# Kernel tuning notes

Hardware: AMD Instinct MI355X
Metric: run time of the kernel (lower is better)

The kernel has to match this reference:

```python
import jax, jax.numpy as jnp
import numpy as np

B, N, IN_DIM, SLOT_DIM, NUM_SLOTS, NUM_ITERS = 64, 4096, 256, 256, 8, 3
LN_EPS = 1e-5


def _ln(x, g, b):
    m = jnp.mean(x, axis=-1, keepdims=True)
    v = jnp.mean(jnp.square(x - m), axis=-1, keepdims=True)
    return (x - m) * jax.lax.rsqrt(v + LN_EPS) * g + b


def setup_inputs() -> dict:
    key = jax.random.key(0)
    ks = jax.random.split(key, 16)
    D, I = SLOT_DIM, IN_DIM
    s = 0.02
    return {
        "inputs": jax.random.normal(ks[0], (B, N, I), jnp.float32),
        "slots_noise": jax.random.normal(ks[1], (B, NUM_SLOTS, D), jnp.float32),
        "slots_mu": jax.random.normal(ks[2], (1, 1, D), jnp.float32),
        "slots_log_sigma": jnp.zeros((1, 1, D), jnp.float32),
        "ln_in_g": jnp.ones((I,), jnp.float32), "ln_in_b": jnp.zeros((I,), jnp.float32),
        "ln_s_g": jnp.ones((D,), jnp.float32), "ln_s_b": jnp.zeros((D,), jnp.float32),
        "ln_m_g": jnp.ones((D,), jnp.float32), "ln_m_b": jnp.zeros((D,), jnp.float32),
        "Wq": jax.random.normal(ks[3], (D, D), jnp.float32) * s,
        "Wk": jax.random.normal(ks[4], (I, D), jnp.float32) * s,
        "Wv": jax.random.normal(ks[5], (I, D), jnp.float32) * s,
        "gru_w_ih": jax.random.normal(ks[6], (3 * D, D), jnp.float32) * s,
        "gru_w_hh": jax.random.normal(ks[7], (3 * D, D), jnp.float32) * s,
        "gru_b_ih": jnp.zeros((3 * D,), jnp.float32),
        "gru_b_hh": jnp.zeros((3 * D,), jnp.float32),
        "mlp_w1": jax.random.normal(ks[8], (D, 4 * D), jnp.float32) * s,
        "mlp_b1": jnp.zeros((4 * D,), jnp.float32),
        "mlp_w2": jax.random.normal(ks[9], (4 * D, D), jnp.float32) * s,
        "mlp_b2": jnp.zeros((D,), jnp.float32),
    }


def reference(inputs, slots_noise, slots_mu, slots_log_sigma, ln_in_g, ln_in_b,
              ln_s_g, ln_s_b, ln_m_g, ln_m_b, Wq, Wk, Wv,
              gru_w_ih, gru_w_hh, gru_b_ih, gru_b_hh,
              mlp_w1, mlp_b1, mlp_w2, mlp_b2):
    D = SLOT_DIM
    # slot init: mu + sigma * noise
    slots = slots_mu + jnp.exp(slots_log_sigma) * slots_noise  # [B, S, D]
    x = _ln(inputs, ln_in_g, ln_in_b)                          # [B, N, I]
    k = x @ Wk                                                 # [B, N, D]
    v = x @ Wv                                                 # [B, N, D]
    scale = 1.0 / jnp.sqrt(jnp.float32(D))
    attn = None
    for _ in range(NUM_ITERS):
        slots_prev = slots
        s_n = _ln(slots, ln_s_g, ln_s_b)
        q = s_n @ Wq                                           # [B, S, D]
        logits = jnp.einsum('bnd,bmd->bnm', k, q) * scale      # [B, N, S]
        attn = jax.nn.softmax(logits, axis=-1)                 # softmax over slots
        attn_nrm = attn / (jnp.sum(attn, axis=1, keepdims=True) + 1e-8)
        updates = jnp.einsum('bnm,bnd->bmd', attn_nrm, v)      # [B, S, D]
        # GRUCell (PyTorch semantics)
        gi = updates @ gru_w_ih.T + gru_b_ih                   # [B, S, 3D]
        gh = slots_prev @ gru_w_hh.T + gru_b_hh
        gi_r, gi_z, gi_n = jnp.split(gi, 3, axis=-1)
        gh_r, gh_z, gh_n = jnp.split(gh, 3, axis=-1)
        r = jax.nn.sigmoid(gi_r + gh_r)
        z = jax.nn.sigmoid(gi_z + gh_z)
        n = jnp.tanh(gi_n + r * gh_n)
        slots = (1.0 - z) * n + z * slots_prev
        # residual MLP
        h = jax.nn.relu(_ln(slots, ln_m_g, ln_m_b) @ mlp_w1 + mlp_b1)
        slots = slots + h @ mlp_w2 + mlp_b2
    return slots, jnp.transpose(attn, (0, 2, 1))
```

## Files before the change

### kernel.cpp

```cpp
#include <hip/hip_runtime.h>


typedef unsigned short u16;
typedef __attribute__((ext_vector_type(8))) short bf16x8;
typedef __attribute__((ext_vector_type(4))) float f32x4;

#define MFMA16(a, b, c) __builtin_amdgcn_mfma_f32_16x16x32_bf16((a), (b), (c), 0, 0, 0)

__device__ __forceinline__ u16 f2bf(float f) {
  union { float f; unsigned u; } v; v.f = f;
  unsigned r = (v.u + 0x7fffu + ((v.u >> 16) & 1u)) >> 16;
  return (u16)r;
}
__device__ __forceinline__ float sigm(float x) { return 1.f / (1.f + __expf(-x)); }
__device__ __forceinline__ float tanh_f(float x) { return 1.f - 2.f / (1.f + __expf(2.f * x)); }

__global__ __launch_bounds__(256) void prep_kernel(
    const float* __restrict__ Wq, const float* __restrict__ Wk, const float* __restrict__ Wv,
    const float* __restrict__ wih, const float* __restrict__ whh,
    const float* __restrict__ w1, const float* __restrict__ w2,
    u16* __restrict__ wkB, u16* __restrict__ wqT, u16* __restrict__ wvT,
    u16* __restrict__ wihB, u16* __restrict__ whhB, u16* __restrict__ w1T, u16* __restrict__ w2T) {
  const int bid = blockIdx.x;
  const int tid = threadIdx.x;
  if (bid < 160) {
    __shared__ float tile[64][65];
    const float* src; u16* dst; int R, C, t;
    if (bid < 16)      { src = Wq; dst = wqT; R = 256;  C = 256;  t = bid; }
    else if (bid < 32) { src = Wv; dst = wvT; R = 256;  C = 256;  t = bid - 16; }
    else if (bid < 96) { src = w1; dst = w1T; R = 1024; C = 256;  t = bid - 32; }
    else               { src = w2; dst = w2T; R = 256;  C = 1024; t = bid - 96; }
    const int tilesJ = C >> 6;
    const int i0 = (t / tilesJ) * 64, j0 = (t % tilesJ) * 64;
    const int c = tid & 63, r0 = tid >> 6;
#pragma unroll
    for (int rr = 0; rr < 16; rr++) {
      int row = rr * 4 + r0;
      tile[row][c] = src[(size_t)(j0 + row) * R + i0 + c];
    }
    __syncthreads();
#pragma unroll
    for (int rr = 0; rr < 16; rr++) {
      int row = rr * 4 + r0;
      dst[(size_t)(i0 + row) * C + j0 + c] = f2bf(tile[c][row]);
    }
  } else {
    int gid = (bid - 160) * 256 + tid;
    for (int i4 = gid; i4 < 114688; i4 += 64 * 256) {
      int i = i4 * 4;
      const float* s; u16* d; int off;
      if (i < 65536) { s = Wk; d = wkB; off = i; }
      else if (i < 262144) { s = wih; d = wihB; off = i - 65536; }
      else { s = whh; d = whhB; off = i - 262144; }
      float4 v = *reinterpret_cast<const float4*>(s + off);
      unsigned lo = (unsigned)f2bf(v.x) | ((unsigned)f2bf(v.y) << 16);
      unsigned hi = (unsigned)f2bf(v.z) | ((unsigned)f2bf(v.w) << 16);
      *reinterpret_cast<uint2*>(d + off) = make_uint2(lo, hi);
    }
  }
}

__device__ __forceinline__ void ln_row16(const float (*src)[264], u16 (*dst)[264],
                                         const float* __restrict__ g, const float* __restrict__ bb,
                                         int wave, int lane) {
  int row = wave;
  if (row < 8) {
    float4 v = *reinterpret_cast<const float4*>(&src[row][lane * 4]);
    float s = v.x + v.y + v.z + v.w;
    float sq = v.x * v.x + v.y * v.y + v.z * v.z + v.w * v.w;
#pragma unroll
    for (int m = 1; m < 64; m <<= 1) { s += __shfl_xor(s, m); sq += __shfl_xor(sq, m); }
    float mu = s * (1.f / 256.f);
    float var = sq * (1.f / 256.f) - mu * mu;
    float rstd = rsqrtf(fmaxf(var, 0.f) + 1e-5f);
    float4 gg = *reinterpret_cast<const float4*>(&g[lane * 4]);
    float4 bv = *reinterpret_cast<const float4*>(&bb[lane * 4]);
    unsigned lo = (unsigned)f2bf((v.x - mu) * rstd * gg.x + bv.x) |
                  ((unsigned)f2bf((v.y - mu) * rstd * gg.y + bv.y) << 16);
    unsigned hi = (unsigned)f2bf((v.z - mu) * rstd * gg.z + bv.z) |
                  ((unsigned)f2bf((v.w - mu) * rstd * gg.w + bv.w) << 16);
    *reinterpret_cast<uint2*>(&dst[row][lane * 4]) = make_uint2(lo, hi);
  } else if (row < 16) {
    *reinterpret_cast<uint2*>(&dst[row][lane * 4]) = make_uint2(0, 0);
  }
}

__global__ __launch_bounds__(1024, 4) void slot_kernel(
    float* __restrict__ slots, u16* __restrict__ qg, float* __restrict__ cd,
    const float* __restrict__ wsY, const float* __restrict__ wsS,
    const u16* __restrict__ wvT, const u16* __restrict__ wihB, const u16* __restrict__ whhB,
    const u16* __restrict__ w1T, const u16* __restrict__ w2T, const u16* __restrict__ wqT,
    const u16* __restrict__ wkB,
    const float* __restrict__ bih, const float* __restrict__ bhh,
    const float* __restrict__ b1v, const float* __restrict__ b2v,
    const float* __restrict__ g_in, const float* __restrict__ b_in,
    const float* __restrict__ g_s, const float* __restrict__ b_s,
    const float* __restrict__ g_m, const float* __restrict__ b_m,
    const float* __restrict__ s_mu, const float* __restrict__ s_ls,
    const float* __restrict__ noise,
    float* __restrict__ d_out, int do_update) {
  __shared__ alignas(16) char pool[58368];
  u16 (*h_lds)[1032] = reinterpret_cast<u16(*)[1032]>(pool);
  u16 (*u_lds)[264] = reinterpret_cast<u16(*)[264]>(pool);
  u16 (*uv_lds)[264] = reinterpret_cast<u16(*)[264]>(pool + 8448);
  u16 (*sb_lds)[264] = reinterpret_cast<u16(*)[264]>(pool + 16896);
  u16 (*m_lds)[264] = reinterpret_cast<u16(*)[264]>(pool + 33024);
  float (*ns_lds)[264] = reinterpret_cast<float(*)[264]>(pool + 41472);
  u16 (*q_lds)[264] = reinterpret_cast<u16(*)[264]>(pool + 41472);
  __shared__ float sS0[16], sS1[16], sInv[16];
  __shared__ float redq[16][4][4][2];

  const int b = blockIdx.x;
  const int tid = threadIdx.x;
  const int lane = tid & 63, wave = tid >> 6;
  const int quad = lane >> 4, col = lane & 15;
  const int i256 = tid & 255, s4 = tid >> 8;
  const f32x4 vzero = {0.f, 0.f, 0.f, 0.f};

  if (do_update) {
    if (tid < 16) {
      float S0 = 0.f, S1 = 0.f;
      if (tid < 8) {
        for (int c = 0; c < 8; c++) {
          S0 += wsS[((b * 8 + c) * 8 + tid) * 2 + 0];
          S1 += wsS[((b * 8 + c) * 8 + tid) * 2 + 1];
        }
      }
      sS0[tid] = S0; sS1[tid] = S1; sInv[tid] = 1.f / (S0 + 1e-8f);
    }
#pragma unroll
    for (int r = 0; r < 4; r++) {
      int s = s4 + r * 4;
      sb_lds[s][i256] = (s < 8) ? f2bf(slots[(size_t)(b * 8 + s) * 256 + i256]) : (u16)0;
    }
    __syncthreads();
    {
      float gv = g_in[i256], bv = b_in[i256];
#pragma unroll
      for (int r = 0; r < 4; r++) {
        int s = s4 + r * 4;
        if (s < 8) {
          float y = 0.f;
#pragma unroll
          for (int c = 0; c < 8; c++) y += wsY[((size_t)((b * 8 + c) * 8 + s)) * 256 + i256];
          u_lds[s][i256] = f2bf((gv * (y - sS1[s]) + bv * sS0[s]) * sInv[s]);
        } else {
          u_lds[s][i256] = 0;
        }
      }
    }
    __syncthreads();
    {
      bf16x8 af[8];
#pragma unroll
      for (int k = 0; k < 8; k++)
        af[k] = *reinterpret_cast<const bf16x8*>(&u_lds[col][k * 32 + quad * 8]);
      int ct = wave;
      f32x4 acc = vzero;
#pragma unroll
      for (int k = 0; k < 8; k++) {
        bf16x8 bf = *reinterpret_cast<const bf16x8*>(wvT + (size_t)(ct * 16 + col) * 256 + k * 32 + quad * 8);
        acc = MFMA16(af[k], bf, acc);
      }
#pragma unroll
      for (int r = 0; r < 4; r++) {
        int s = quad * 4 + r;
        uv_lds[s][ct * 16 + col] = (s < 8) ? f2bf(acc[r]) : (u16)0;
      }
    }
    __syncthreads();
    {
      bf16x8 afu[8], afs[8];
#pragma unroll
      for (int k = 0; k < 8; k++) {
        afu[k] = *reinterpret_cast<const bf16x8*>(&uv_lds[col][k * 32 + quad * 8]);
        afs[k] = *reinterpret_cast<const bf16x8*>(&sb_lds[col][k * 32 + quad * 8]);
      }
      int d = wave * 16 + col;
      f32x4 a_ir = vzero, a_iz = vzero, a_in = vzero, a_hr = vzero, a_hz = vzero, a_hn = vzero;
#pragma unroll
      for (int k = 0; k < 8; k++) {
        int ko = k * 32 + quad * 8;
        a_ir = MFMA16(afu[k], *reinterpret_cast<const bf16x8*>(wihB + (size_t)(d)*256 + ko), a_ir);
        a_iz = MFMA16(afu[k], *reinterpret_cast<const bf16x8*>(wihB + (size_t)(256 + d) * 256 + ko), a_iz);
        a_in = MFMA16(afu[k], *reinterpret_cast<const bf16x8*>(wihB + (size_t)(512 + d) * 256 + ko), a_in);
        a_hr = MFMA16(afs[k], *reinterpret_cast<const bf16x8*>(whhB + (size_t)(d)*256 + ko), a_hr);
        a_hz = MFMA16(afs[k], *reinterpret_cast<const bf16x8*>(whhB + (size_t)(256 + d) * 256 + ko), a_hz);
        a_hn = MFMA16(afs[k], *reinterpret_cast<const bf16x8*>(whhB + (size_t)(512 + d) * 256 + ko), a_hn);
      }
      float bihr = bih[d], bihz = bih[256 + d], bihn = bih[512 + d];
      float bhhr = bhh[d], bhhz = bhh[256 + d], bhhn = bhh[512 + d];
#pragma unroll
      for (int r = 0; r < 4; r++) {
        int s = quad * 4 + r;
        float rg = sigm(a_ir[r] + bihr + a_hr[r] + bhhr);
        float zg = sigm(a_iz[r] + bihz + a_hz[r] + bhhz);
        float ng = tanh_f(a_in[r] + bihn + rg * (a_hn[r] + bhhn));
        float prev = (s < 8) ? slots[(size_t)(b * 8 + s) * 256 + d] : 0.f;
        float ns = (1.f - zg) * ng + zg * prev;
        ns_lds[s][d] = (s < 8) ? ns : 0.f;
      }
    }
    __syncthreads();
    ln_row16(ns_lds, m_lds, g_m, b_m, wave, lane);
    __syncthreads();
    {
      bf16x8 af[8];
#pragma unroll
      for (int k = 0; k < 8; k++)
        af[k] = *reinterpret_cast<const bf16x8*>(&m_lds[col][k * 32 + quad * 8]);
      for (int cc = 0; cc < 4; cc++) {
        int ct = wave * 4 + cc;
        f32x4 acc = vzero;
#pragma unroll
        for (int k = 0; k < 8; k++) {
          bf16x8 bf = *reinterpret_cast<const bf16x8*>(w1T + (size_t)(ct * 16 + col) * 256 + k * 32 + quad * 8);
          acc = MFMA16(af[k], bf, acc);
        }
        float bb = b1v[ct * 16 + col];
#pragma unroll
        for (int r = 0; r < 4; r++) {
          int s = quad * 4 + r;
          float h = fmaxf(acc[r] + bb, 0.f);
          h_lds[s][ct * 16 + col] = (s < 8) ? f2bf(h) : (u16)0;
        }
      }
    }
    __syncthreads();
    {
      int ct = wave;
      f32x4 acc = vzero;
      for (int k = 0; k < 32; k++) {
        bf16x8 af = *reinterpret_cast<const bf16x8*>(&h_lds[col][k * 32 + quad * 8]);
        bf16x8 bf = *reinterpret_cast<const bf16x8*>(w2T + (size_t)(ct * 16 + col) * 1024 + k * 32 + quad * 8);
        acc = MFMA16(af, bf, acc);
      }
      int d = ct * 16 + col;
      float bb = b2v[d];
#pragma unroll
      for (int r = 0; r < 4; r++) {
        int s = quad * 4 + r;
        if (s < 8) {
          float fin = ns_lds[s][d] + acc[r] + bb;
          slots[(size_t)(b * 8 + s) * 256 + d] = fin;
          d_out[(size_t)(b * 8 + s) * 256 + d] = fin;
          ns_lds[s][d] = fin;
        }
      }
    }
    __syncthreads();
  } else {
#pragma unroll
    for (int r = 0; r < 4; r++) {
      int s = s4 + r * 4;
      float v = 0.f;
      if (s < 8) {
        v = s_mu[i256] + __expf(s_ls[i256]) * noise[(size_t)(b * 8 + s) * 256 + i256];
        slots[(size_t)(b * 8 + s) * 256 + i256] = v;
      }
      ns_lds[s][i256] = v;
    }
    __syncthreads();
  }

  ln_row16(ns_lds, m_lds, g_s, b_s, wave, lane);
  __syncthreads();
  {
    bf16x8 af[8];
#pragma unroll
    for (int k = 0; k < 8; k++)
      af[k] = *reinterpret_cast<const bf16x8*>(&m_lds[col][k * 32 + quad * 8]);
    int ct = wave;
    f32x4 acc = vzero;
#pragma unroll
    for (int k = 0; k < 8; k++) {
      bf16x8 bf = *reinterpret_cast<const bf16x8*>(wqT + (size_t)(ct * 16 + col) * 256 + k * 32 + quad * 8);
      acc = MFMA16(af[k], bf, acc);
    }
#pragma unroll
    for (int r = 0; r < 4; r++) {
      int s = quad * 4 + r;
      q_lds[s][ct * 16 + col] = (s < 8) ? f2bf(acc[r]) : (u16)0;
    }
  }
  __syncthreads();
  {
    bf16x8 af[8];
#pragma unroll
    for (int k = 0; k < 8; k++)
      af[k] = *reinterpret_cast<const bf16x8*>(&q_lds[col][k * 32 + quad * 8]);
    float cacc[4] = {0.f, 0.f, 0.f, 0.f}, dacc[4] = {0.f, 0.f, 0.f, 0.f};
    int ct = wave;
    f32x4 acc = vzero;
#pragma unroll
    for (int k = 0; k < 8; k++) {
      bf16x8 bf = *reinterpret_cast<const bf16x8*>(wkB + (size_t)(ct * 16 + col) * 256 + k * 32 + quad * 8);
      acc = MFMA16(af[k], bf, acc);
    }
    int i = ct * 16 + col;
    float gi_ = g_in[i] * 0.0625f, bi_ = b_in[i] * 0.0625f;
#pragma unroll
    for (int r = 0; r < 4; r++) {
      int s = quad * 4 + r;
      float qkv = acc[r];
      float qgv = (s < 8) ? gi_ * qkv : 0.f;
      qg[(size_t)(b * 16 + s) * 256 + i] = f2bf(qgv);
      cacc[r] -= qgv;
      dacc[r] += (s < 8) ? bi_ * qkv : 0.f;
    }
#pragma unroll
    for (int r = 0; r < 4; r++) {
#pragma unroll
      for (int m = 1; m < 16; m <<= 1) {
        cacc[r] += __shfl_xor(cacc[r], m);
        dacc[r] += __shfl_xor(dacc[r], m);
      }
    }
    if (col == 0) {
#pragma unroll
      for (int r = 0; r < 4; r++) {
        redq[wave][quad][r][0] = cacc[r];
        redq[wave][quad][r][1] = dacc[r];
      }
    }
    __syncthreads();
    if (tid < 16) {
      int qd = tid >> 2, r = tid & 3;
      float c = 0.f, dd = 0.f;
      for (int w = 0; w < 16; w++) { c += redq[w][qd][r][0]; dd += redq[w][qd][r][1]; }
      cd[(b * 16 + tid) * 2 + 0] = c;
      cd[(b * 16 + tid) * 2 + 1] = dd;
    }
  }
}

template <int PASS>
__global__ __launch_bounds__(512, 4) void attn_kernel(
    const float* __restrict__ x, u16* __restrict__ xb, float2* __restrict__ stats2,
    const u16* __restrict__ qg, const float* __restrict__ cd,
    float* __restrict__ out, float* __restrict__ wsY, float* __restrict__ wsS) {
  __shared__ alignas(16) u16 x_lds[64][264];
  __shared__ alignas(16) u16 a2t[16][72];
  __shared__ float2 stats_lds[64];
  __shared__ float2 red2[4][8];

  const int chunk = blockIdx.x, b = blockIdx.y;
  const int tid = threadIdx.x;
  const int lane = tid & 63, wave = tid >> 6;
  const int quad = lane >> 4, col = lane & 15;

  for (int idx = tid; idx < 288; idx += 512)
    reinterpret_cast<unsigned*>(&a2t[8][0])[idx] = 0;

  bf16x8 bfrag[8];
#pragma unroll
  for (int k = 0; k < 8; k++)
    bfrag[k] = *reinterpret_cast<const bf16x8*>(qg + (size_t)(b * 16 + col) * 256 + k * 32 + quad * 8);
  const float2 cdv = *reinterpret_cast<const float2*>(cd + (b * 16 + col) * 2);

  f32x4 Yacc[2];
  Yacc[0] = {0.f, 0.f, 0.f, 0.f};
  Yacc[1] = {0.f, 0.f, 0.f, 0.f};
  float s0a = 0.f, s1a = 0.f;
  float* out_attn = out + 131072;

  float4 pf0[8];
  uint2 pf1[8];
  float2 pfs;
  {
    const int nb0 = chunk * 512;
    if (PASS == 0) {
#pragma unroll
      for (int p = 0; p < 8; p++)
        pf0[p] = *reinterpret_cast<const float4*>(x + (size_t)(b * 4096 + nb0 + wave * 8 + p) * 256 + lane * 4);
    } else {
#pragma unroll
      for (int p = 0; p < 8; p++)
        pf1[p] = *reinterpret_cast<const uint2*>(xb + (size_t)(b * 4096 + nb0 + wave * 8 + p) * 256 + lane * 4);
      if (tid < 64) pfs = stats2[(size_t)b * 4096 + nb0 + tid];
    }
  }

  for (int g = 0; g < 8; g++) {
    const int nb = chunk * 512 + g * 64;
    __syncthreads();
    if (PASS == 0) {
#pragma unroll
      for (int p = 0; p < 8; p++) {
        int row = wave * 8 + p;
        float4 v = pf0[p];
        float s = v.x + v.y + v.z + v.w;
        float sq = v.x * v.x + v.y * v.y + v.z * v.z + v.w * v.w;
#pragma unroll
        for (int m = 1; m < 64; m <<= 1) { s += __shfl_xor(s, m); sq += __shfl_xor(sq, m); }
        float mu = s * (1.f / 256.f);
        float var = sq * (1.f / 256.f) - mu * mu;
        float rstd = rsqrtf(fmaxf(var, 0.f) + 1e-5f);
        float2 st = make_float2(rstd, rstd * mu);
        if (lane == 0) {
          stats_lds[row] = st;
          stats2[(size_t)b * 4096 + nb + row] = st;
        }
        unsigned lo = (unsigned)f2bf(v.x) | ((unsigned)f2bf(v.y) << 16);
        unsigned hi = (unsigned)f2bf(v.z) | ((unsigned)f2bf(v.w) << 16);
        *reinterpret_cast<uint2*>(&x_lds[row][lane * 4]) = make_uint2(lo, hi);
        *reinterpret_cast<uint2*>(xb + (size_t)(b * 4096 + nb + row) * 256 + lane * 4) = make_uint2(lo, hi);
      }
    } else {
#pragma unroll
      for (int p = 0; p < 8; p++) {
        int row = wave * 8 + p;
        *reinterpret_cast<uint2*>(&x_lds[row][lane * 4]) = pf1[p];
      }
      if (tid < 64) stats_lds[tid] = pfs;
    }
    __syncthreads();
    if (g < 7) {
      const int nbn = nb + 64;
      if (PASS == 0) {
#pragma unroll
        for (int p = 0; p < 8; p++)
          pf0[p] = *reinterpret_cast<const float4*>(x + (size_t)(b * 4096 + nbn + wave * 8 + p) * 256 + lane * 4);
      } else {
#pragma unroll
        for (int p = 0; p < 8; p++)
          pf1[p] = *reinterpret_cast<const uint2*>(xb + (size_t)(b * 4096 + nbn + wave * 8 + p) * 256 + lane * 4);
        if (tid < 64) pfs = stats2[(size_t)b * 4096 + nbn + tid];
      }
    }
    if (wave < 4) {
      const int rowbase = wave * 16;
      f32x4 acc = {0.f, 0.f, 0.f, 0.f};
#pragma unroll
      for (int k = 0; k < 8; k++) {
        bf16x8 af = *reinterpret_cast<const bf16x8*>(&x_lds[rowbase + col][k * 32 + quad * 8]);
        acc = MFMA16(af, bfrag[k], acc);
      }
      float at[4], rmx[4], rmy[4];
#pragma unroll
      for (int r = 0; r < 4; r++) {
        float2 rm = stats_lds[rowbase + quad * 4 + r];
        rmx[r] = rm.x; rmy[r] = rm.y;
        float lg = rm.x * acc[r] + rm.y * cdv.x + cdv.y;
        float mx = lg;
        mx = fmaxf(mx, __shfl_xor(mx, 1));
        mx = fmaxf(mx, __shfl_xor(mx, 2));
        mx = fmaxf(mx, __shfl_xor(mx, 4));
        float e = __expf(lg - mx);
        float sm = e;
        sm += __shfl_xor(sm, 1); sm += __shfl_xor(sm, 2); sm += __shfl_xor(sm, 4);
        at[r] = e / sm;
      }
      if (col < 8) {
#pragma unroll
        for (int r = 0; r < 4; r++) {
          int n_loc = rowbase + quad * 4 + r;
          out_attn[(size_t)(b * 8 + col) * 4096 + nb + n_loc] = at[r];
          a2t[col][n_loc] = f2bf(at[r] * rmx[r]);
          s0a += at[r];
          s1a += at[r] * rmy[r];
        }
      }
    }
    __syncthreads();
    {
      bf16x8 af0 = *reinterpret_cast<const bf16x8*>(&a2t[col][quad * 8]);
      bf16x8 af1 = *reinterpret_cast<const bf16x8*>(&a2t[col][32 + quad * 8]);
#pragma unroll
      for (int cc = 0; cc < 2; cc++) {
        int ib = (wave * 2 + cc) * 16 + col;
        union { short s[8]; bf16x8 v; } b0, b1;
#pragma unroll
        for (int j = 0; j < 8; j++) {
          b0.s[j] = (short)x_lds[quad * 8 + j][ib];
          b1.s[j] = (short)x_lds[32 + quad * 8 + j][ib];
        }
        Yacc[cc] = MFMA16(af0, b0.v, Yacc[cc]);
        Yacc[cc] = MFMA16(af1, b1.v, Yacc[cc]);
      }
    }
  }
  if (quad < 2) {
#pragma unroll
    for (int cc = 0; cc < 2; cc++) {
      int i = (wave * 2 + cc) * 16 + col;
#pragma unroll
      for (int r = 0; r < 4; r++) {
        int s = quad * 4 + r;
        wsY[(size_t)((b * 8 + chunk) * 8 + s) * 256 + i] = Yacc[cc][r];
      }
    }
  }
  s0a += __shfl_xor(s0a, 16); s0a += __shfl_xor(s0a, 32);
  s1a += __shfl_xor(s1a, 16); s1a += __shfl_xor(s1a, 32);
  if (wave < 4 && lane < 8) red2[wave][lane] = make_float2(s0a, s1a);
  __syncthreads();
  if (tid < 8) {
    float S0 = 0.f, S1 = 0.f;
#pragma unroll
    for (int w = 0; w < 4; w++) { S0 += red2[w][tid].x; S1 += red2[w][tid].y; }
    wsS[((b * 8 + chunk) * 8 + tid) * 2 + 0] = S0;
    wsS[((b * 8 + chunk) * 8 + tid) * 2 + 1] = S1;
  }
}

extern "C" void kernel_launch(void* const* d_in, const int* in_sizes, int n_in,
                              void* d_out, int out_size, void* d_ws, size_t ws_size,
                              hipStream_t stream) {
  const float* inputs = (const float*)d_in[0];
  const float* noise = (const float*)d_in[1];
  const float* s_mu = (const float*)d_in[2];
  const float* s_ls = (const float*)d_in[3];
  const float* g_in = (const float*)d_in[4];
  const float* b_in = (const float*)d_in[5];
  const float* g_s = (const float*)d_in[6];
  const float* b_s = (const float*)d_in[7];
  const float* g_m = (const float*)d_in[8];
  const float* b_m = (const float*)d_in[9];
  const float* Wq = (const float*)d_in[10];
  const float* Wk = (const float*)d_in[11];
  const float* Wv = (const float*)d_in[12];
  const float* wih = (const float*)d_in[13];
  const float* whh = (const float*)d_in[14];
  const float* bih = (const float*)d_in[15];
  const float* bhh = (const float*)d_in[16];
  const float* w1 = (const float*)d_in[17];
  const float* b1v = (const float*)d_in[18];
  const float* w2 = (const float*)d_in[19];
  const float* b2v = (const float*)d_in[20];
  float* out = (float*)d_out;

  size_t o = 0;
  auto take = [&](size_t bytes) {
    void* p = (char*)d_ws + o;
    o += (bytes + 255) & ~(size_t)255;
    return p;
  };
  float* slots = (float*)take((size_t)64 * 8 * 256 * 4);
  u16* qg = (u16*)take((size_t)64 * 16 * 256 * 2);
  float* cd = (float*)take((size_t)64 * 16 * 2 * 4);
  float* wsY = (float*)take((size_t)64 * 8 * 8 * 256 * 4);
  float* wsS = (float*)take((size_t)64 * 8 * 8 * 2 * 4);
  u16* wkB = (u16*)take((size_t)65536 * 2);
  u16* wqT = (u16*)take((size_t)65536 * 2);
  u16* wvT = (u16*)take((size_t)65536 * 2);
  u16* wihB = (u16*)take((size_t)196608 * 2);
  u16* whhB = (u16*)take((size_t)196608 * 2);
  u16* w1T = (u16*)take((size_t)262144 * 2);
  u16* w2T = (u16*)take((size_t)262144 * 2);
  u16* xb = (u16*)take((size_t)64 * 4096 * 256 * 2);
  float2* stats2 = (float2*)take((size_t)64 * 4096 * 8);

  prep_kernel<<<224, 256, 0, stream>>>(Wq, Wk, Wv, wih, whh, w1, w2,
                                       wkB, wqT, wvT, wihB, whhB, w1T, w2T);
  slot_kernel<<<64, 1024, 0, stream>>>(slots, qg, cd, wsY, wsS,
                                       wvT, wihB, whhB, w1T, w2T, wqT, wkB,
                                       bih, bhh, b1v, b2v,
                                       g_in, b_in, g_s, b_s, g_m, b_m,
                                       s_mu, s_ls, noise, out, 0);
  for (int it = 0; it < 3; it++) {
    if (it == 0)
      attn_kernel<0><<<dim3(8, 64), 512, 0, stream>>>(inputs, xb, stats2, qg, cd, out, wsY, wsS);
    else
      attn_kernel<1><<<dim3(8, 64), 512, 0, stream>>>(inputs, xb, stats2, qg, cd, out, wsY, wsS);
    slot_kernel<<<64, 1024, 0, stream>>>(slots, qg, cd, wsY, wsS,
                                         wvT, wihB, whhB, w1T, w2T, wqT, wkB,
                                         bih, bhh, b1v, b2v,
                                         g_in, b_in, g_s, b_s, g_m, b_m,
                                         s_mu, s_ls, noise, out, 1);
  }
}
```

Baseline: 701.9 us.

## Split attention into smaller 256-thread blocks with redundant per-wave logits and MFMA LayerNorm stats

Reworks the attention kernel into 32 chunks of 128 rows per batch, using 256-thread blocks with 32-row tiles. Every wave redundantly computes the logits and softmax for the tile so that each wave owns its own attention slice and accumulates a different quarter of the output columns, which removes the cross-wave barrier and reduction. In pass 0, row mean and variance are computed with MFMA against a ones vector and an x·x Gram diagonal instead of shuffle reductions. The register prefetch of the next tile is dropped, and the slot kernel now reduces 32 partial results instead of 8, giving more blocks for occupancy at the cost of redundant MFMA work and a larger workspace.

```diff
diff --git a/kernel.cpp b/kernel.cpp
--- a/kernel.cpp
+++ b/kernel.cpp
@@ -121,9 +121,9 @@
     if (tid < 16) {
       float S0 = 0.f, S1 = 0.f;
       if (tid < 8) {
-        for (int c = 0; c < 8; c++) {
-          S0 += wsS[((b * 8 + c) * 8 + tid) * 2 + 0];
-          S1 += wsS[((b * 8 + c) * 8 + tid) * 2 + 1];
+        for (int c = 0; c < 32; c++) {
+          S0 += wsS[((b * 32 + c) * 8 + tid) * 2 + 0];
+          S1 += wsS[((b * 32 + c) * 8 + tid) * 2 + 1];
         }
       }
       sS0[tid] = S0; sS1[tid] = S1; sInv[tid] = 1.f / (S0 + 1e-8f);
@@ -142,7 +142,7 @@
         if (s < 8) {
           float y = 0.f;
 #pragma unroll
-          for (int c = 0; c < 8; c++) y += wsY[((size_t)((b * 8 + c) * 8 + s)) * 256 + i256];
+          for (int c = 0; c < 32; c++) y += wsY[((size_t)((b * 32 + c) * 8 + s)) * 256 + i256];
           u_lds[s][i256] = f2bf((gv * (y - sS1[s]) + bv * sS0[s]) * sInv[s]);
         } else {
           u_lds[s][i256] = 0;
@@ -335,72 +335,35 @@
 }
 
 template <int PASS>
-__global__ __launch_bounds__(512, 4) void attn_kernel(
+__global__ __launch_bounds__(256, 5) void attn_kernel(
     const float* __restrict__ x, u16* __restrict__ xb, float2* __restrict__ stats2,
     const u16* __restrict__ qg, const float* __restrict__ cd,
     float* __restrict__ out, float* __restrict__ wsY, float* __restrict__ wsS) {
-  __shared__ alignas(16) u16 x_lds[64][264];
-  __shared__ alignas(16) u16 a2t[16][72];
-  __shared__ float2 stats_lds[64];
-  __shared__ float2 red2[4][8];
+  __shared__ alignas(16) u16 x_lds[32][280];
+  __shared__ alignas(16) u16 a2s[4][16][40];
+  __shared__ float2 stats_lds[32];
 
   const int chunk = blockIdx.x, b = blockIdx.y;
   const int tid = threadIdx.x;
   const int lane = tid & 63, wave = tid >> 6;
   const int quad = lane >> 4, col = lane & 15;
 
-  for (int idx = tid; idx < 288; idx += 512)
-    reinterpret_cast<unsigned*>(&a2t[8][0])[idx] = 0;
-
-  bf16x8 bfrag[8];
-#pragma unroll
-  for (int k = 0; k < 8; k++)
-    bfrag[k] = *reinterpret_cast<const bf16x8*>(qg + (size_t)(b * 16 + col) * 256 + k * 32 + quad * 8);
   const float2 cdv = *reinterpret_cast<const float2*>(cd + (b * 16 + col) * 2);
 
-  f32x4 Yacc[2];
-  Yacc[0] = {0.f, 0.f, 0.f, 0.f};
-  Yacc[1] = {0.f, 0.f, 0.f, 0.f};
+  f32x4 Yacc[4];
+#pragma unroll
+  for (int cc = 0; cc < 4; cc++) Yacc[cc] = {0.f, 0.f, 0.f, 0.f};
   float s0a = 0.f, s1a = 0.f;
   float* out_attn = out + 131072;
 
-  float4 pf0[8];
-  uint2 pf1[8];
-  float2 pfs;
-  {
-    const int nb0 = chunk * 512;
+  for (int g = 0; g < 4; g++) {
+    const int nb = chunk * 128 + g * 32;
+    __syncthreads();
     if (PASS == 0) {
 #pragma unroll
-      for (int p = 0; p < 8; p++)
-        pf0[p] = *reinterpret_cast<const float4*>(x + (size_t)(b * 4096 + nb0 + wave * 8 + p) * 256 + lane * 4);
-    } else {
-#pragma unroll
-      for (int p = 0; p < 8; p++)
-        pf1[p] = *reinterpret_cast<const uint2*>(xb + (size_t)(b * 4096 + nb0 + wave * 8 + p) * 256 + lane * 4);
-      if (tid < 64) pfs = stats2[(size_t)b * 4096 + nb0 + tid];
-    }
-  }
-
-  for (int g = 0; g < 8; g++) {
-    const int nb = chunk * 512 + g * 64;
-    __syncthreads();
-    if (PASS == 0) {
-#pragma unroll
       for (int p = 0; p < 8; p++) {
-        int row = wave * 8 + p;
-        float4 v = pf0[p];
-        float s = v.x + v.y + v.z + v.w;
-        float sq = v.x * v.x + v.y * v.y + v.z * v.z + v.w * v.w;
-#pragma unroll
-        for (int m = 1; m < 64; m <<= 1) { s += __shfl_xor(s, m); sq += __shfl_xor(sq, m); }
-        float mu = s * (1.f / 256.f);
-        float var = sq * (1.f / 256.f) - mu * mu;
-        float rstd = rsqrtf(fmaxf(var, 0.f) + 1e-5f);
-        float2 st = make_float2(rstd, rstd * mu);
-        if (lane == 0) {
-          stats_lds[row] = st;
-          stats2[(size_t)b * 4096 + nb + row] = st;
-        }
+        const int row = wave * 8 + p;
+        float4 v = *reinterpret_cast<const float4*>(x + (size_t)(b * 4096 + nb + row) * 256 + lane * 4);
         unsigned lo = (unsigned)f2bf(v.x) | ((unsigned)f2bf(v.y) << 16);
         unsigned hi = (unsigned)f2bf(v.z) | ((unsigned)f2bf(v.w) << 16);
         *reinterpret_cast<uint2*>(&x_lds[row][lane * 4]) = make_uint2(lo, hi);
@@ -409,39 +372,62 @@
     } else {
 #pragma unroll
       for (int p = 0; p < 8; p++) {
-        int row = wave * 8 + p;
-        *reinterpret_cast<uint2*>(&x_lds[row][lane * 4]) = pf1[p];
-      }
-      if (tid < 64) stats_lds[tid] = pfs;
-    }
-    __syncthreads();
-    if (g < 7) {
-      const int nbn = nb + 64;
+        const int row = wave * 8 + p;
+        *reinterpret_cast<uint2*>(&x_lds[row][lane * 4]) =
+            *reinterpret_cast<const uint2*>(xb + (size_t)(b * 4096 + nb + row) * 256 + lane * 4);
+      }
+      if (tid < 32) stats_lds[tid] = stats2[(size_t)b * 4096 + nb + tid];
+    }
+    __syncthreads();
+
+    bf16x8 bfrag[8];
+#pragma unroll
+    for (int k = 0; k < 8; k++)
+      bfrag[k] = *reinterpret_cast<const bf16x8*>(qg + (size_t)(b * 16 + col) * 256 + k * 32 + quad * 8);
+#pragma unroll
+    for (int t = 0; t < 2; t++) {
+      bf16x8 af[8];
+#pragma unroll
+      for (int k = 0; k < 8; k++)
+        af[k] = *reinterpret_cast<const bf16x8*>(&x_lds[t * 16 + col][k * 32 + quad * 8]);
+      f32x4 acc = {0.f, 0.f, 0.f, 0.f};
+#pragma unroll
+      for (int k = 0; k < 8; k++) acc = MFMA16(af[k], bfrag[k], acc);
+
+      float rmx[4], rmy[4];
       if (PASS == 0) {
-#pragma unroll
-        for (int p = 0; p < 8; p++)
-          pf0[p] = *reinterpret_cast<const float4*>(x + (size_t)(b * 4096 + nbn + wave * 8 + p) * 256 + lane * 4);
+        const short one_bf = (short)0x3F80;
+        bf16x8 ones8 = {one_bf, one_bf, one_bf, one_bf, one_bf, one_bf, one_bf, one_bf};
+        f32x4 accS = {0.f, 0.f, 0.f, 0.f}, accG = {0.f, 0.f, 0.f, 0.f};
+#pragma unroll
+        for (int k = 0; k < 8; k++) {
+          accS = MFMA16(af[k], ones8, accS);
+          accG = MFMA16(af[k], af[k], accG);
+        }
+#pragma unroll
+        for (int r = 0; r < 4; r++) {
+          float sq = __shfl(accG[r], (quad << 4) + quad * 4 + r);
+          float mu = accS[r] * (1.f / 256.f);
+          float var = sq * (1.f / 256.f) - mu * mu;
+          float rstd = rsqrtf(fmaxf(var, 0.f) + 1e-5f);
+          rmx[r] = rstd; rmy[r] = rstd * mu;
+        }
+        if (wave == 0 && col == 0) {
+#pragma unroll
+          for (int r = 0; r < 4; r++)
+            stats2[(size_t)b * 4096 + nb + t * 16 + quad * 4 + r] = make_float2(rmx[r], rmy[r]);
+        }
       } else {
 #pragma unroll
-        for (int p = 0; p < 8; p++)
-          pf1[p] = *reinterpret_cast<const uint2*>(xb + (size_t)(b * 4096 + nbn + wave * 8 + p) * 256 + lane * 4);
-        if (tid < 64) pfs = stats2[(size_t)b * 4096 + nbn + tid];
-      }
-    }
-    if (wave < 4) {
-      const int rowbase = wave * 16;
-      f32x4 acc = {0.f, 0.f, 0.f, 0.f};
-#pragma unroll
-      for (int k = 0; k < 8; k++) {
-        bf16x8 af = *reinterpret_cast<const bf16x8*>(&x_lds[rowbase + col][k * 32 + quad * 8]);
-        acc = MFMA16(af, bfrag[k], acc);
-      }
-      float at[4], rmx[4], rmy[4];
-#pragma unroll
-      for (int r = 0; r < 4; r++) {
-        float2 rm = stats_lds[rowbase + quad * 4 + r];
-        rmx[r] = rm.x; rmy[r] = rm.y;
-        float lg = rm.x * acc[r] + rm.y * cdv.x + cdv.y;
+        for (int r = 0; r < 4; r++) {
+          float2 rm = stats_lds[t * 16 + quad * 4 + r];
+          rmx[r] = rm.x; rmy[r] = rm.y;
+        }
+      }
+      float at[4];
+#pragma unroll
+      for (int r = 0; r < 4; r++) {
+        float lg = rmx[r] * acc[r] + rmy[r] * cdv.x + cdv.y;
         float mx = lg;
         mx = fmaxf(mx, __shfl_xor(mx, 1));
         mx = fmaxf(mx, __shfl_xor(mx, 2));
@@ -453,54 +439,46 @@
       }
       if (col < 8) {
 #pragma unroll
-        for (int r = 0; r < 4; r++) {
-          int n_loc = rowbase + quad * 4 + r;
-          out_attn[(size_t)(b * 8 + col) * 4096 + nb + n_loc] = at[r];
-          a2t[col][n_loc] = f2bf(at[r] * rmx[r]);
-          s0a += at[r];
-          s1a += at[r] * rmy[r];
-        }
-      }
-    }
-    __syncthreads();
+        for (int r = 0; r < 4; r++)
+          a2s[wave][col][t * 16 + quad * 4 + r] = f2bf(at[r] * rmx[r]);
+        if (wave == 0) {
+#pragma unroll
+          for (int r = 0; r < 4; r++) {
+            out_attn[(size_t)(b * 8 + col) * 4096 + nb + t * 16 + quad * 4 + r] = at[r];
+            s0a += at[r];
+            s1a += at[r] * rmy[r];
+          }
+        }
+      }
+    }
     {
-      bf16x8 af0 = *reinterpret_cast<const bf16x8*>(&a2t[col][quad * 8]);
-      bf16x8 af1 = *reinterpret_cast<const bf16x8*>(&a2t[col][32 + quad * 8]);
-#pragma unroll
-      for (int cc = 0; cc < 2; cc++) {
-        int ib = (wave * 2 + cc) * 16 + col;
-        union { short s[8]; bf16x8 v; } b0, b1;
-#pragma unroll
-        for (int j = 0; j < 8; j++) {
-          b0.s[j] = (short)x_lds[quad * 8 + j][ib];
-          b1.s[j] = (short)x_lds[32 + quad * 8 + j][ib];
-        }
-        Yacc[cc] = MFMA16(af0, b0.v, Yacc[cc]);
-        Yacc[cc] = MFMA16(af1, b1.v, Yacc[cc]);
+      bf16x8 afa = *reinterpret_cast<const bf16x8*>(&a2s[wave][col][quad * 8]);
+#pragma unroll
+      for (int cc = 0; cc < 4; cc++) {
+        const int ib = (wave * 4 + cc) * 16 + col;
+        union { short s[8]; bf16x8 v; } bx;
+#pragma unroll
+        for (int j = 0; j < 8; j++) bx.s[j] = (short)x_lds[quad * 8 + j][ib];
+        Yacc[cc] = MFMA16(afa, bx.v, Yacc[cc]);
       }
     }
   }
   if (quad < 2) {
 #pragma unroll
-    for (int cc = 0; cc < 2; cc++) {
-      int i = (wave * 2 + cc) * 16 + col;
+    for (int cc = 0; cc < 4; cc++) {
+      int i = (wave * 4 + cc) * 16 + col;
 #pragma unroll
       for (int r = 0; r < 4; r++) {
         int s = quad * 4 + r;
-        wsY[(size_t)((b * 8 + chunk) * 8 + s) * 256 + i] = Yacc[cc][r];
+        wsY[(size_t)((b * 32 + chunk) * 8 + s) * 256 + i] = Yacc[cc][r];
       }
     }
   }
   s0a += __shfl_xor(s0a, 16); s0a += __shfl_xor(s0a, 32);
   s1a += __shfl_xor(s1a, 16); s1a += __shfl_xor(s1a, 32);
-  if (wave < 4 && lane < 8) red2[wave][lane] = make_float2(s0a, s1a);
-  __syncthreads();
-  if (tid < 8) {
-    float S0 = 0.f, S1 = 0.f;
-#pragma unroll
-    for (int w = 0; w < 4; w++) { S0 += red2[w][tid].x; S1 += red2[w][tid].y; }
-    wsS[((b * 8 + chunk) * 8 + tid) * 2 + 0] = S0;
-    wsS[((b * 8 + chunk) * 8 + tid) * 2 + 1] = S1;
+  if (wave == 0 && lane < 8) {
+    wsS[((b * 32 + chunk) * 8 + lane) * 2 + 0] = s0a;
+    wsS[((b * 32 + chunk) * 8 + lane) * 2 + 1] = s1a;
   }
 }
 
@@ -539,8 +517,8 @@
   float* slots = (float*)take((size_t)64 * 8 * 256 * 4);
   u16* qg = (u16*)take((size_t)64 * 16 * 256 * 2);
   float* cd = (float*)take((size_t)64 * 16 * 2 * 4);
-  float* wsY = (float*)take((size_t)64 * 8 * 8 * 256 * 4);
-  float* wsS = (float*)take((size_t)64 * 8 * 8 * 2 * 4);
+  float* wsY = (float*)take((size_t)64 * 32 * 8 * 256 * 4);
+  float* wsS = (float*)take((size_t)64 * 32 * 8 * 2 * 4);
   u16* wkB = (u16*)take((size_t)65536 * 2);
   u16* wqT = (u16*)take((size_t)65536 * 2);
   u16* wvT = (u16*)take((size_t)65536 * 2);
@@ -560,9 +538,9 @@
                                        s_mu, s_ls, noise, out, 0);
   for (int it = 0; it < 3; it++) {
     if (it == 0)
-      attn_kernel<0><<<dim3(8, 64), 512, 0, stream>>>(inputs, xb, stats2, qg, cd, out, wsY, wsS);
+      attn_kernel<0><<<dim3(32, 64), 256, 0, stream>>>(inputs, xb, stats2, qg, cd, out, wsY, wsS);
     else
-      attn_kernel<1><<<dim3(8, 64), 512, 0, stream>>>(inputs, xb, stats2, qg, cd, out, wsY, wsS);
+      attn_kernel<1><<<dim3(32, 64), 256, 0, stream>>>(inputs, xb, stats2, qg, cd, out, wsY, wsS);
     slot_kernel<<<64, 1024, 0, stream>>>(slots, qg, cd, wsY, wsS,
                                          wvT, wihB, whhB, w1T, w2T, wqT, wkB,
                                          bih, bhh, b1v, b2v,
```

After: 808.2 us. 1.15x slower.
